# Performance work log

Hardware: AMD Instinct MI355X
Metric: run time of the kernel (lower is better)

The kernel has to match this reference:

```python
import jax, jax.numpy as jnp
import numpy as np


def _silu(x):
    return x * jax.nn.sigmoid(x)


def _mamba_dir(h, W_in, conv_w, conv_b, Wx, Wdt, bdt, A_log, Dp, W_out):
    """One unidirectional Mamba (v1) block. h: [B, L, Dm] -> [B, L, Dm]."""
    Bsz, L, Dm = h.shape
    Di = W_in.shape[0] // 2
    N = A_log.shape[1]
    K = conv_w.shape[1]
    dt_rank = Wdt.shape[1]
    # input projection -> x, z gates
    xz = jnp.einsum('bld,ed->ble', h, W_in)  # [B, L, 2*Di]
    x, z = xz[..., :Di], xz[..., Di:]
    # causal depthwise conv over time
    xc = jnp.transpose(x, (0, 2, 1))  # [B, Di, L]
    xc = jax.lax.conv_general_dilated(
        xc, conv_w[:, None, :], window_strides=(1,), padding=[(K - 1, 0)],
        dimension_numbers=('NCH', 'OIH', 'NCH'), feature_group_count=Di)
    x = _silu(jnp.transpose(xc, (0, 2, 1)) + conv_b[None, None, :])  # [B, L, Di]
    # data-dependent dt, B, C
    x_dbl = jnp.einsum('bld,ed->ble', x, Wx)  # [B, L, dt_rank + 2N]
    dt = x_dbl[..., :dt_rank]
    Bm = x_dbl[..., dt_rank:dt_rank + N]      # [B, L, N]
    Cm = x_dbl[..., dt_rank + N:]             # [B, L, N]
    dt = jax.nn.softplus(jnp.einsum('blr,dr->bld', dt, Wdt) + bdt)  # [B, L, Di]
    A = -jnp.exp(A_log)                       # [Di, N]
    # ZOH discretization
    dA = jnp.exp(dt[..., None] * A)                     # [B, L, Di, N]
    dBx = (dt * x)[..., None] * Bm[:, :, None, :]       # [B, L, Di, N]

    def step(hc, inp):
        dA_t, dBx_t, C_t = inp
        hc = dA_t * hc + dBx_t                          # [B, Di, N]
        return hc, jnp.einsum('bdn,bn->bd', hc, C_t)

    h0 = jnp.zeros((Bsz, Di, N), dtype=x.dtype)
    _, ys = jax.lax.scan(step, h0, (jnp.moveaxis(dA, 1, 0),
                                    jnp.moveaxis(dBx, 1, 0),
                                    jnp.moveaxis(Cm, 1, 0)))
    y = jnp.moveaxis(ys, 0, 1) + x * Dp                  # [B, L, Di]
    y = y * _silu(z)
    return jnp.einsum('bld,ed->ble', y, W_out)           # [B, L, Dm]


def setup_inputs() -> dict:
    key = jax.random.key(0)
    ks = jax.random.split(key, 16)
    B, L, Dm = 1, 2048, 1024
    Di, N, Kc, R = 2048, 16, 4, 64
    s = 0.02
    inp = {
        'hidden_states': jax.random.normal(ks[0], (B, L, Dm), jnp.float32),
        'W_in':  jax.random.normal(ks[1], (2 * Di, Dm), jnp.float32) * s,
        'W_out': jax.random.normal(ks[2], (Dm, Di), jnp.float32) * s,
    }
    a_log = jnp.log(jnp.broadcast_to(jnp.arange(1, N + 1, dtype=jnp.float32), (Di, N)))
    for i, d in enumerate(['fwd', 'rev']):
        o = 3 + 6 * i
        inp[f'conv_w_{d}'] = jax.random.normal(ks[o + 0], (Di, Kc), jnp.float32) * 0.2
        inp[f'conv_b_{d}'] = jnp.zeros((Di,), jnp.float32)
        inp[f'Wx_{d}']     = jax.random.normal(ks[o + 1], (R + 2 * N, Di), jnp.float32) * s
        inp[f'Wdt_{d}']    = jax.random.normal(ks[o + 2], (Di, R), jnp.float32) * s
        inp[f'bdt_{d}']    = jnp.full((Di,), -4.6, jnp.float32)  # softplus ~ 0.01
        inp[f'A_log_{d}']  = a_log
        inp[f'D_{d}']      = jnp.ones((Di,), jnp.float32)
    return inp


def reference(hidden_states, W_in, W_out,
              conv_w_fwd, conv_b_fwd, Wx_fwd, Wdt_fwd, bdt_fwd, A_log_fwd, D_fwd,
              conv_w_rev, conv_b_rev, Wx_rev, Wdt_rev, bdt_rev, A_log_rev, D_rev):
    out = _mamba_dir(hidden_states, W_in, conv_w_fwd, conv_b_fwd, Wx_fwd,
                     Wdt_fwd, bdt_fwd, A_log_fwd, D_fwd, W_out)
    h_rev = jnp.flip(hidden_states, axis=-2)
    out_rev = _mamba_dir(h_rev, W_in, conv_w_rev, conv_b_rev, Wx_rev,
                         Wdt_rev, bdt_rev, A_log_rev, D_rev, W_out)
    return out + jnp.flip(out_rev, axis=-2)
```

## Files before the change

### kernel.cpp

```cpp
#include <hip/hip_runtime.h>

#define L_LEN 2048
#define DM 1024
#define DI 2048
#define NS 16
#define KC 4
#define RR 64
#define XS 128
#define SPK 8
#define CH2 128
#define TCH2 (L_LEN / CH2)

typedef __attribute__((ext_vector_type(8))) short bf16x8;
typedef __attribute__((ext_vector_type(4))) float f32x4;

__device__ __forceinline__ float silu_f(float v) { return v / (1.f + __expf(-v)); }

__device__ __forceinline__ float exp2_f(float x) {
  float r;
  asm("v_exp_f32 %0, %1" : "=v"(r) : "v"(x));
  return r;
}

__device__ __forceinline__ unsigned short f2bf(float f) {
  unsigned int u = __float_as_uint(f);
  u = (u + 0x7FFFu + ((u >> 16) & 1u)) >> 16;
  return (unsigned short)u;
}
__device__ __forceinline__ float bf2f(unsigned short u) {
  return __uint_as_float((unsigned int)u << 16);
}

#define GLOAD_LDS16(gptr, lptr)                                                \
  __builtin_amdgcn_global_load_lds(                                            \
      (const __attribute__((address_space(1))) void*)(gptr),                   \
      (__attribute__((address_space(3))) void*)(lptr), 16, 0, 0)

template <int BM, int EPI, int KSPLIT>
__global__ __launch_bounds__(256) void gemm_bf16(
    const unsigned short* __restrict__ A, const unsigned short* __restrict__ B,
    void* __restrict__ Cv, void* __restrict__ Cv2, int M, int N, int K,
    size_t zsA, size_t zsB, size_t zsC,
    const float* __restrict__ biasf, const float* __restrict__ biasr)
{
  constexpr int MF = BM / 32;
  constexpr int WM = BM / 2;
  A += (size_t)blockIdx.z * zsA;
  B += (size_t)blockIdx.z * zsB;
  __shared__ unsigned short smem[(BM + 128) * 32];
  unsigned short* As = smem;
  unsigned short* Bs = smem + BM * 32;
  const int tid = threadIdx.x;
  const int wid = tid >> 6;
  const int lane = tid & 63;
  const int bm = blockIdx.x * BM;
  const int bn = (KSPLIT > 1) ? 0 : blockIdx.y * 128;
  int kbeg = 0, kend = K;
  if (KSPLIT > 1) {
    int kl = K / KSPLIT;
    kbeg = blockIdx.y * kl; kend = kbeg + kl;
  }
  const int wm = wid >> 1, wn = wid & 1;
  const int arow = tid >> 2;
  const int swz_kel = (((tid & 3) ^ ((tid >> 3) & 3)) << 3);
  const int qa = (((lane >> 4) ^ ((lane >> 1) & 3)) << 4);
  const int frow = lane & 15;

  f32x4 acc[MF][4];
#pragma unroll
  for (int mi = 0; mi < MF; ++mi)
#pragma unroll
    for (int ni = 0; ni < 4; ++ni) acc[mi][ni] = 0.f;

  const unsigned short* Ab = A + (size_t)bm * K + swz_kel;
  const unsigned short* Bb = B + (size_t)bn * K + swz_kel;

  for (int k0 = kbeg; k0 < kend; k0 += 32) {
#pragma unroll
    for (int i = 0; i < BM / 64; ++i)
      GLOAD_LDS16(Ab + (size_t)(i * 64 + arow) * K + k0,
                  (char*)As + i * 4096 + wid * 1024);
#pragma unroll
    for (int i = 0; i < 2; ++i)
      GLOAD_LDS16(Bb + (size_t)(i * 64 + arow) * K + k0,
                  (char*)Bs + i * 4096 + wid * 1024);
    __syncthreads();
    bf16x8 af[MF], bfr[4];
#pragma unroll
    for (int mi = 0; mi < MF; ++mi)
      af[mi] = *(const bf16x8*)((const char*)As + (wm * WM + mi * 16 + frow) * 64 + qa);
#pragma unroll
    for (int ni = 0; ni < 4; ++ni)
      bfr[ni] = *(const bf16x8*)((const char*)Bs + (wn * 64 + ni * 16 + frow) * 64 + qa);
#pragma unroll
    for (int mi = 0; mi < MF; ++mi)
#pragma unroll
      for (int ni = 0; ni < 4; ++ni)
        acc[mi][ni] = __builtin_amdgcn_mfma_f32_16x16x32_bf16(
            af[mi], bfr[ni], acc[mi][ni], 0, 0, 0);
    __syncthreads();
  }
  const int crow0 = bm + wm * WM + ((lane >> 4) << 2);
  const int ccol0 = bn + wn * 64 + frow;
  if (EPI == 1) {
    unsigned short* Cu = (unsigned short*)Cv + (size_t)blockIdx.z * zsC;
    const float* bias = blockIdx.z ? biasr : biasf;
    float bn4[4];
#pragma unroll
    for (int ni = 0; ni < 4; ++ni) bn4[ni] = bias[ccol0 + ni * 16];
#pragma unroll
    for (int mi = 0; mi < MF; ++mi)
#pragma unroll
      for (int ni = 0; ni < 4; ++ni)
#pragma unroll
        for (int v = 0; v < 4; ++v) {
          float val = acc[mi][ni][v] + bn4[ni];
          float sp = (val > 20.f) ? val : __logf(1.f + __expf(val));
          Cu[(size_t)(crow0 + mi * 16 + v) * N + ccol0 + ni * 16] = f2bf(sp);
        }
  } else if (EPI == 2) {
    unsigned short* Co = (bn < DI) ? (unsigned short*)Cv : (unsigned short*)Cv2;
    const int cbase = (bn < DI) ? 0 : DI;
#pragma unroll
    for (int mi = 0; mi < MF; ++mi)
#pragma unroll
      for (int ni = 0; ni < 4; ++ni)
#pragma unroll
        for (int v = 0; v < 4; ++v)
          Co[(size_t)(crow0 + mi * 16 + v) * DI + ccol0 + ni * 16 - cbase] =
              f2bf(acc[mi][ni][v]);
  } else {
    float* Cf = (float*)Cv + (size_t)blockIdx.z * zsC;
    if (KSPLIT > 1) Cf += (size_t)blockIdx.y * 2 * M * 128;
#pragma unroll
    for (int mi = 0; mi < MF; ++mi)
#pragma unroll
      for (int ni = 0; ni < 4; ++ni)
#pragma unroll
        for (int v = 0; v < 4; ++v)
          Cf[(size_t)(crow0 + mi * 16 + v) * N + ccol0 + ni * 16] = acc[mi][ni][v];
  }
}

__global__ __launch_bounds__(256) void cast_all(
    const float* __restrict__ Wxf, const float* __restrict__ Wxr,
    const float* __restrict__ Wdtf, const float* __restrict__ Wdtr,
    const float* __restrict__ W_out, const float* __restrict__ h,
    const float* __restrict__ W_in,
    unsigned short* __restrict__ Wxpad, unsigned short* __restrict__ wdtb,
    unsigned short* __restrict__ wob, unsigned short* __restrict__ hb)
{
  int idx = (blockIdx.x * 256 + threadIdx.x) * 4;
  const int N0 = 2 * XS * DI;
  const int N1 = N0 + 2 * DI * RR;
  const int N2 = N1 + DM * DI;
  const int N3 = N2 + L_LEN * DM;
  float4 v;
  ushort4 o = {0, 0, 0, 0};
  if (idx < N0) {
    int dir = idx >> 18;
    int rem = idx & ((1 << 18) - 1);
    int row = rem >> 11;
    if (row < 96) {
      v = *(const float4*)((dir ? Wxr : Wxf) + (size_t)row * DI + (rem & (DI - 1)));
      o.x = f2bf(v.x); o.y = f2bf(v.y); o.z = f2bf(v.z); o.w = f2bf(v.w);
    }
    *(ushort4*)(Wxpad + idx) = o;
    return;
  }
  unsigned short* dst;
  const float* src;
  int j;
  if (idx < N1)      { j = idx - N0; int dir = j >> 17;
                       src = (dir ? Wdtr : Wdtf) + (j & ((1 << 17) - 1)); dst = wdtb + j; }
  else if (idx < N2) { j = idx - N1; src = W_out + j; dst = wob + j; }
  else if (idx < N3) { j = idx - N2; src = h + j;     dst = hb + j; }
  else               { j = idx - N3; src = W_in + j;  dst = hb + (L_LEN * DM) + j; }
  v = *(const float4*)src;
  o.x = f2bf(v.x); o.y = f2bf(v.y); o.z = f2bf(v.z); o.w = f2bf(v.w);
  *(ushort4*)dst = o;
}

__global__ __launch_bounds__(256) void xdbl_reduce2(
    const float* __restrict__ part, float* __restrict__ xdbl2,
    unsigned short* __restrict__ xdblb)
{
  int idx = (blockIdx.x * 256 + threadIdx.x) * 4;
  f32x4 s = {0.f, 0.f, 0.f, 0.f};
#pragma unroll
  for (int sp = 0; sp < SPK; ++sp) {
    f32x4 p = *(const f32x4*)(part + (size_t)sp * 2 * L_LEN * XS + idx);
#pragma unroll
    for (int j = 0; j < 4; ++j) s[j] += p[j];
  }
  *(f32x4*)(xdbl2 + idx) = s;
  int col = idx & (XS - 1);
  if (col < RR) {
    int dr = idx >> 7;
    ushort4 o;
    o.x = f2bf(s[0]); o.y = f2bf(s[1]); o.z = f2bf(s[2]); o.w = f2bf(s[3]);
    *(ushort4*)(xdblb + (size_t)dr * RR + col) = o;
  }
}

__global__ __launch_bounds__(256) void conv_silu4(
    const unsigned short* __restrict__ xb,
    const float* __restrict__ wf, const float* __restrict__ bf,
    const float* __restrict__ wr, const float* __restrict__ br,
    unsigned short* __restrict__ xob)
{
  const int dir = blockIdx.y;
  const int idx = (blockIdx.x * 256 + threadIdx.x) * 4;
  const int d = idx & (DI - 1);
  const int t = idx >> 11;
  const float* w = dir ? wr : wf;
  const float* bb = dir ? br : bf;
  f32x4 wq[4];
#pragma unroll
  for (int j = 0; j < 4; ++j) wq[j] = *(const f32x4*)(w + (d + j) * KC);
  f32x4 s = {0.f, 0.f, 0.f, 0.f};
#pragma unroll
  for (int k = 0; k < KC; ++k) {
    int tt = t - (KC - 1) + k;
    if (tt >= 0) {
      int row = dir ? (L_LEN - 1 - tt) : tt;
      ushort4 xv = *(const ushort4*)(xb + (size_t)row * DI + d);
      s[0] = fmaf(wq[0][k], bf2f(xv.x), s[0]);
      s[1] = fmaf(wq[1][k], bf2f(xv.y), s[1]);
      s[2] = fmaf(wq[2][k], bf2f(xv.z), s[2]);
      s[3] = fmaf(wq[3][k], bf2f(xv.w), s[3]);
    }
  }
  f32x4 bv = *(const f32x4*)(bb + d);
  ushort4 o;
  o.x = f2bf(silu_f(s[0] + bv[0])); o.y = f2bf(silu_f(s[1] + bv[1]));
  o.z = f2bf(silu_f(s[2] + bv[2])); o.w = f2bf(silu_f(s[3] + bv[3]));
  *(ushort4*)(xob + (size_t)dir * L_LEN * DI + idx) = o;
}

__global__ __launch_bounds__(256) void scan_partial2(
    const unsigned short* __restrict__ dtb16, const unsigned short* __restrict__ xwb,
    const float* __restrict__ xdbl2,
    const float* __restrict__ Alogf, const float* __restrict__ Alogr,
    float* __restrict__ hch, float* __restrict__ sdtb)
{
  const int dir = blockIdx.z, c = blockIdx.y;
  const int d = blockIdx.x * 256 + threadIdx.x;
  const int t0 = c * TCH2;
  const unsigned short* dtp = dtb16 + (size_t)dir * L_LEN * DI + (size_t)t0 * DI + d;
  const unsigned short* xp  = xwb   + (size_t)dir * L_LEN * DI + (size_t)t0 * DI + d;
  const float* xdp = xdbl2 + (size_t)dir * L_LEN * XS + (size_t)t0 * XS;
  const float* Alog = (dir ? Alogr : Alogf) + (size_t)d * NS;
  f32x4 a4[4], h4[4];
#pragma unroll
  for (int g = 0; g < 4; ++g) {
    f32x4 al = *(const f32x4*)(Alog + g * 4);
#pragma unroll
    for (int j = 0; j < 4; ++j) a4[g][j] = -__expf(al[j]) * 1.44269504f;
    h4[g] = 0.f;
  }
  float sdt = 0.f;
#pragma unroll
  for (int tt = 0; tt < TCH2; ++tt) {
    float dtv = bf2f(*dtp);
    float xv  = bf2f(*xp);
    float dtx = dtv * xv;
    sdt += dtv;
#pragma unroll
    for (int g = 0; g < 4; ++g) {
      f32x4 Bv = *(const f32x4*)(xdp + RR + g * 4);
#pragma unroll
      for (int j = 0; j < 4; ++j)
        h4[g][j] = fmaf(exp2_f(dtv * a4[g][j]), h4[g][j], dtx * Bv[j]);
    }
    dtp += DI; xp += DI; xdp += XS;
  }
  float* hp = hch + ((((size_t)c * 2 + dir) * 4) * DI + d) * 4;
#pragma unroll
  for (int g = 0; g < 4; ++g) *(f32x4*)(hp + (size_t)g * DI * 4) = h4[g];
  sdtb[((size_t)c * 2 + dir) * DI + d] = sdt;
}

__global__ __launch_bounds__(256) void scan_combine2(
    float* __restrict__ hch, const float* __restrict__ sdtb,
    const float* __restrict__ Alogf, const float* __restrict__ Alogr)
{
  const int idx = blockIdx.x * 256 + threadIdx.x;
  const int dir = idx / (DI * NS);
  const int rem = idx - dir * (DI * NS);
  const int d = rem >> 4, n = rem & 15;
  const float* Alog = dir ? Alogr : Alogf;
  const float A2 = -__expf(Alog[rem]) * 1.44269504f;
  float H = 0.f;
  for (int c = 0; c < CH2; ++c) {
    size_t off = ((((size_t)c * 2 + dir) * 4 + (n >> 2)) * DI + d) * 4 + (n & 3);
    float hc = hch[off];
    hch[off] = H;
    H = fmaf(exp2_f(A2 * sdtb[((size_t)c * 2 + dir) * DI + d]), H, hc);
  }
}

__global__ __launch_bounds__(256) void scan_final3(
    const unsigned short* __restrict__ dtb16, const unsigned short* __restrict__ xwb,
    const float* __restrict__ xdbl2,
    const float* __restrict__ Alogf, const float* __restrict__ Alogr,
    const float* __restrict__ Df, const float* __restrict__ Dr,
    const float* __restrict__ Hin, const unsigned short* __restrict__ zb,
    unsigned short* __restrict__ yb)
{
  const int c = blockIdx.y;
  const int d = blockIdx.x * 256 + threadIdx.x;
  float ur[TCH2];
  {
    const int cr = CH2 - 1 - c;
    const int tr0 = cr * TCH2;
    const unsigned short* dtp = dtb16 + (size_t)L_LEN * DI + (size_t)tr0 * DI + d;
    const unsigned short* xp  = xwb   + (size_t)L_LEN * DI + (size_t)tr0 * DI + d;
    const float* xdp = xdbl2 + (size_t)L_LEN * XS + (size_t)tr0 * XS;
    const float* Alog = Alogr + (size_t)d * NS;
    const float Dp = Dr[d];
    f32x4 a4[4], h4[4];
#pragma unroll
    for (int g = 0; g < 4; ++g) {
      f32x4 al = *(const f32x4*)(Alog + g * 4);
      h4[g] = *(const f32x4*)(Hin + ((((size_t)cr * 2 + 1) * 4 + g) * DI + d) * 4);
#pragma unroll
      for (int j = 0; j < 4; ++j) a4[g][j] = -__expf(al[j]) * 1.44269504f;
    }
#pragma unroll
    for (int s = 0; s < TCH2; ++s) {
      float dtv = bf2f(*dtp);
      float xv  = bf2f(*xp);
      float dtx = dtv * xv;
      f32x4 p4 = {0.f, 0.f, 0.f, 0.f};
#pragma unroll
      for (int g = 0; g < 4; ++g) {
        f32x4 Bv = *(const f32x4*)(xdp + RR + g * 4);
        f32x4 Cv = *(const f32x4*)(xdp + RR + NS + g * 4);
#pragma unroll
        for (int j = 0; j < 4; ++j) {
          h4[g][j] = fmaf(exp2_f(dtv * a4[g][j]), h4[g][j], dtx * Bv[j]);
          p4[j] = fmaf(h4[g][j], Cv[j], p4[j]);
        }
      }
      float p = (p4[0] + p4[1]) + (p4[2] + p4[3]);
      ur[s] = fmaf(xv, Dp, p);
      dtp += DI; xp += DI; xdp += XS;
    }
  }
  {
    const int t0 = c * TCH2;
    const unsigned short* dtp = dtb16 + (size_t)t0 * DI + d;
    const unsigned short* xp  = xwb   + (size_t)t0 * DI + d;
    const float* xdp = xdbl2 + (size_t)t0 * XS;
    const unsigned short* zp = zb + (size_t)t0 * DI + d;
    unsigned short* yp = yb + (size_t)t0 * DI + d;
    const float* Alog = Alogf + (size_t)d * NS;
    const float Dp = Df[d];
    f32x4 a4[4], h4[4];
#pragma unroll
    for (int g = 0; g < 4; ++g) {
      f32x4 al = *(const f32x4*)(Alog + g * 4);
      h4[g] = *(const f32x4*)(Hin + ((((size_t)c * 2 + 0) * 4 + g) * DI + d) * 4);
#pragma unroll
      for (int j = 0; j < 4; ++j) a4[g][j] = -__expf(al[j]) * 1.44269504f;
    }
#pragma unroll
    for (int tt = 0; tt < TCH2; ++tt) {
      float dtv = bf2f(*dtp);
      float xv  = bf2f(*xp);
      float dtx = dtv * xv;
      f32x4 p4 = {0.f, 0.f, 0.f, 0.f};
#pragma unroll
      for (int g = 0; g < 4; ++g) {
        f32x4 Bv = *(const f32x4*)(xdp + RR + g * 4);
        f32x4 Cv = *(const f32x4*)(xdp + RR + NS + g * 4);
#pragma unroll
        for (int j = 0; j < 4; ++j) {
          h4[g][j] = fmaf(exp2_f(dtv * a4[g][j]), h4[g][j], dtx * Bv[j]);
          p4[j] = fmaf(h4[g][j], Cv[j], p4[j]);
        }
      }
      float p = (p4[0] + p4[1]) + (p4[2] + p4[3]);
      float uf = fmaf(xv, Dp, p);
      float u = uf + ur[TCH2 - 1 - tt];
      float z = bf2f(*zp);
      *yp = f2bf(u * silu_f(z));
      dtp += DI; xp += DI; xdp += XS; zp += DI; yp += DI;
    }
  }
}

extern "C" void kernel_launch(void* const* d_in, const int* in_sizes, int n_in,
                              void* d_out, int out_size, void* d_ws, size_t ws_size,
                              hipStream_t stream)
{
  const float* h     = (const float*)d_in[0];
  const float* W_in  = (const float*)d_in[1];
  const float* W_out = (const float*)d_in[2];
  const float* cwf   = (const float*)d_in[3];
  const float* cbf   = (const float*)d_in[4];
  const float* Wxf   = (const float*)d_in[5];
  const float* Wdtf  = (const float*)d_in[6];
  const float* bdtf  = (const float*)d_in[7];
  const float* Alogf = (const float*)d_in[8];
  const float* Df    = (const float*)d_in[9];
  const float* cwr   = (const float*)d_in[10];
  const float* cbr   = (const float*)d_in[11];
  const float* Wxr   = (const float*)d_in[12];
  const float* Wdtr  = (const float*)d_in[13];
  const float* bdtr  = (const float*)d_in[14];
  const float* Alogr = (const float*)d_in[15];
  const float* Dr    = (const float*)d_in[16];

  float* ws = (float*)d_ws;
  size_t o = 0;
  float* xb_f    = ws + o; o += (size_t)L_LEN * DI / 2;
  float* zb_f    = ws + o; o += (size_t)L_LEN * DI / 2;
  float* xwb_f   = ws + o; o += (size_t)L_LEN * DI;
  float* dtb_f   = ws + o; o += (size_t)L_LEN * DI;
  float* xdbl2   = ws + o; o += 2ull * L_LEN * XS;
  float* xdblb_f = ws + o; o += (size_t)L_LEN * RR;
  float* wdtb_f  = ws + o; o += (size_t)DI * RR;
  float* Wxpad_f = ws + o; o += (size_t)XS * DI;
  float* wob_f   = ws + o; o += (size_t)DM * DI / 2;
  float* yb_f    = ws + o; o += (size_t)L_LEN * DI / 2;
  float* R0      = ws + o; o += 8912896;
  if (ws_size < o * sizeof(float)) return;

  unsigned short* xb    = (unsigned short*)xb_f;
  unsigned short* zb    = (unsigned short*)zb_f;
  unsigned short* xwb   = (unsigned short*)xwb_f;
  unsigned short* dtb16 = (unsigned short*)dtb_f;
  unsigned short* xdblb = (unsigned short*)xdblb_f;
  unsigned short* wdtb  = (unsigned short*)wdtb_f;
  unsigned short* Wxpad = (unsigned short*)Wxpad_f;
  unsigned short* wob   = (unsigned short*)wob_f;
  unsigned short* yb    = (unsigned short*)yb_f;

  unsigned short* hb   = (unsigned short*)R0;
  float*          part = R0;
  float*          hch  = R0;
  float*          sdtb = R0 + 8388608;

  cast_all<<<(2 * XS * DI + 2 * DI * RR + DM * DI + L_LEN * DM + 2 * DI * DM) / 1024,
             256, 0, stream>>>(
      Wxf, Wxr, Wdtf, Wdtr, W_out, h, W_in, Wxpad, wdtb, wob, hb);

  gemm_bf16<128, 2, 1><<<dim3(L_LEN / 128, (2 * DI) / 128, 1), 256, 0, stream>>>(
      hb, hb + (size_t)L_LEN * DM, xb, zb, L_LEN, 2 * DI, DM, 0, 0, 0,
      nullptr, nullptr);

  conv_silu4<<<dim3(L_LEN * DI / 1024, 2), 256, 0, stream>>>(
      xb, cwf, cbf, cwr, cbr, xwb);

  gemm_bf16<128, 0, SPK><<<dim3(L_LEN / 128, SPK, 2), 256, 0, stream>>>(
      xwb, Wxpad, part, nullptr, L_LEN, XS, DI,
      (size_t)L_LEN * DI, (size_t)XS * DI, (size_t)L_LEN * XS,
      nullptr, nullptr);
  xdbl_reduce2<<<(2 * L_LEN * XS) / 1024, 256, 0, stream>>>(part, xdbl2, xdblb);

  gemm_bf16<128, 1, 1><<<dim3(L_LEN / 128, DI / 128, 2), 256, 0, stream>>>(
      xdblb, wdtb, dtb16, nullptr, L_LEN, DI, RR,
      (size_t)L_LEN * RR, (size_t)DI * RR, (size_t)L_LEN * DI,
      bdtf, bdtr);

  scan_partial2<<<dim3(DI / 256, CH2, 2), 256, 0, stream>>>(
      dtb16, xwb, xdbl2, Alogf, Alogr, hch, sdtb);
  scan_combine2<<<(2 * DI * NS) / 256, 256, 0, stream>>>(
      hch, sdtb, Alogf, Alogr);
  scan_final3<<<dim3(DI / 256, CH2, 1), 256, 0, stream>>>(
      dtb16, xwb, xdbl2, Alogf, Alogr, Df, Dr, hch, zb, yb);

  gemm_bf16<64, 0, 1><<<dim3(L_LEN / 64, DM / 128, 1), 256, 0, stream>>>(
      yb, wob, (float*)d_out, nullptr, L_LEN, DM, DI, 0, 0, 0, nullptr, nullptr);
}
```

Measured before the change: 192.9 us.

## Double-buffer GEMM LDS tiles and store split-K partials and chunk states in bf16

```diff
diff --git a/kernel.cpp b/kernel.cpp
--- a/kernel.cpp
+++ b/kernel.cpp
@@ -45,11 +45,10 @@
 {
   constexpr int MF = BM / 32;
   constexpr int WM = BM / 2;
+  constexpr int HALF = (BM + 128) * 32;
   A += (size_t)blockIdx.z * zsA;
   B += (size_t)blockIdx.z * zsB;
-  __shared__ unsigned short smem[(BM + 128) * 32];
-  unsigned short* As = smem;
-  unsigned short* Bs = smem + BM * 32;
+  __shared__ unsigned short smem[2 * HALF];
   const int tid = threadIdx.x;
   const int wid = tid >> 6;
   const int lane = tid & 63;
@@ -60,6 +59,7 @@
     int kl = K / KSPLIT;
     kbeg = blockIdx.y * kl; kend = kbeg + kl;
   }
+  const int nsteps = (kend - kbeg) >> 5;
   const int wm = wid >> 1, wn = wid & 1;
   const int arow = tid >> 2;
   const int swz_kel = (((tid & 3) ^ ((tid >> 3) & 3)) << 3);
@@ -75,30 +75,44 @@
   const unsigned short* Ab = A + (size_t)bm * K + swz_kel;
   const unsigned short* Bb = B + (size_t)bn * K + swz_kel;
 
-  for (int k0 = kbeg; k0 < kend; k0 += 32) {
+  auto STAGE = [&](int s, int buf) {
+    char* As = (char*)(smem + buf * HALF);
+    char* Bs = As + BM * 64;
+    const int k0 = kbeg + s * 32;
 #pragma unroll
     for (int i = 0; i < BM / 64; ++i)
       GLOAD_LDS16(Ab + (size_t)(i * 64 + arow) * K + k0,
-                  (char*)As + i * 4096 + wid * 1024);
+                  As + i * 4096 + wid * 1024);
 #pragma unroll
     for (int i = 0; i < 2; ++i)
       GLOAD_LDS16(Bb + (size_t)(i * 64 + arow) * K + k0,
-                  (char*)Bs + i * 4096 + wid * 1024);
-    __syncthreads();
+                  Bs + i * 4096 + wid * 1024);
+  };
+
+  STAGE(0, 0);
+  __syncthreads();
+  int cur = 0;
+  for (int s = 0; s < nsteps; ++s) {
+    if (s + 1 < nsteps) STAGE(s + 1, cur ^ 1);
+    const char* As = (const char*)(smem + cur * HALF);
+    const char* Bs = As + BM * 64;
     bf16x8 af[MF], bfr[4];
 #pragma unroll
     for (int mi = 0; mi < MF; ++mi)
-      af[mi] = *(const bf16x8*)((const char*)As + (wm * WM + mi * 16 + frow) * 64 + qa);
+      af[mi] = *(const bf16x8*)(As + (wm * WM + mi * 16 + frow) * 64 + qa);
 #pragma unroll
     for (int ni = 0; ni < 4; ++ni)
-      bfr[ni] = *(const bf16x8*)((const char*)Bs + (wn * 64 + ni * 16 + frow) * 64 + qa);
+      bfr[ni] = *(const bf16x8*)(Bs + (wn * 64 + ni * 16 + frow) * 64 + qa);
 #pragma unroll
     for (int mi = 0; mi < MF; ++mi)
 #pragma unroll
       for (int ni = 0; ni < 4; ++ni)
         acc[mi][ni] = __builtin_amdgcn_mfma_f32_16x16x32_bf16(
             af[mi], bfr[ni], acc[mi][ni], 0, 0, 0);
-    __syncthreads();
+    if (s + 1 < nsteps) {
+      __syncthreads();
+      cur ^= 1;
+    }
   }
   const int crow0 = bm + wm * WM + ((lane >> 4) << 2);
   const int ccol0 = bn + wn * 64 + frow;
@@ -129,9 +143,19 @@
         for (int v = 0; v < 4; ++v)
           Co[(size_t)(crow0 + mi * 16 + v) * DI + ccol0 + ni * 16 - cbase] =
               f2bf(acc[mi][ni][v]);
+  } else if (EPI == 3) {
+    unsigned short* Cu = (unsigned short*)Cv + (size_t)blockIdx.z * zsC +
+                         (size_t)blockIdx.y * 2 * M * 128;
+#pragma unroll
+    for (int mi = 0; mi < MF; ++mi)
+#pragma unroll
+      for (int ni = 0; ni < 4; ++ni)
+#pragma unroll
+        for (int v = 0; v < 4; ++v)
+          Cu[(size_t)(crow0 + mi * 16 + v) * N + ccol0 + ni * 16] =
+              f2bf(acc[mi][ni][v]);
   } else {
     float* Cf = (float*)Cv + (size_t)blockIdx.z * zsC;
-    if (KSPLIT > 1) Cf += (size_t)blockIdx.y * 2 * M * 128;
 #pragma unroll
     for (int mi = 0; mi < MF; ++mi)
 #pragma unroll
@@ -182,16 +206,15 @@
 }
 
 __global__ __launch_bounds__(256) void xdbl_reduce2(
-    const float* __restrict__ part, float* __restrict__ xdbl2,
+    const unsigned short* __restrict__ part, float* __restrict__ xdbl2,
     unsigned short* __restrict__ xdblb)
 {
   int idx = (blockIdx.x * 256 + threadIdx.x) * 4;
   f32x4 s = {0.f, 0.f, 0.f, 0.f};
 #pragma unroll
   for (int sp = 0; sp < SPK; ++sp) {
-    f32x4 p = *(const f32x4*)(part + (size_t)sp * 2 * L_LEN * XS + idx);
-#pragma unroll
-    for (int j = 0; j < 4; ++j) s[j] += p[j];
+    ushort4 p = *(const ushort4*)(part + (size_t)sp * 2 * L_LEN * XS + idx);
+    s[0] += bf2f(p.x); s[1] += bf2f(p.y); s[2] += bf2f(p.z); s[3] += bf2f(p.w);
   }
   *(f32x4*)(xdbl2 + idx) = s;
   int col = idx & (XS - 1);
@@ -242,7 +265,7 @@
     const unsigned short* __restrict__ dtb16, const unsigned short* __restrict__ xwb,
     const float* __restrict__ xdbl2,
     const float* __restrict__ Alogf, const float* __restrict__ Alogr,
-    float* __restrict__ hch, float* __restrict__ sdtb)
+    unsigned short* __restrict__ hch, float* __restrict__ sdtb)
 {
   const int dir = blockIdx.z, c = blockIdx.y;
   const int d = blockIdx.x * 256 + threadIdx.x;
@@ -275,14 +298,19 @@
     }
     dtp += DI; xp += DI; xdp += XS;
   }
-  float* hp = hch + ((((size_t)c * 2 + dir) * 4) * DI + d) * 4;
-#pragma unroll
-  for (int g = 0; g < 4; ++g) *(f32x4*)(hp + (size_t)g * DI * 4) = h4[g];
+  unsigned short* hp = hch + ((((size_t)c * 2 + dir) * 4) * DI + d) * 4;
+#pragma unroll
+  for (int g = 0; g < 4; ++g) {
+    ushort4 o;
+    o.x = f2bf(h4[g][0]); o.y = f2bf(h4[g][1]);
+    o.z = f2bf(h4[g][2]); o.w = f2bf(h4[g][3]);
+    *(ushort4*)(hp + (size_t)g * DI * 4) = o;
+  }
   sdtb[((size_t)c * 2 + dir) * DI + d] = sdt;
 }
 
 __global__ __launch_bounds__(256) void scan_combine2(
-    float* __restrict__ hch, const float* __restrict__ sdtb,
+    unsigned short* __restrict__ hch, const float* __restrict__ sdtb,
     const float* __restrict__ Alogf, const float* __restrict__ Alogr)
 {
   const int idx = blockIdx.x * 256 + threadIdx.x;
@@ -294,8 +322,8 @@
   float H = 0.f;
   for (int c = 0; c < CH2; ++c) {
     size_t off = ((((size_t)c * 2 + dir) * 4 + (n >> 2)) * DI + d) * 4 + (n & 3);
-    float hc = hch[off];
-    hch[off] = H;
+    float hc = bf2f(hch[off]);
+    hch[off] = f2bf(H);
     H = fmaf(exp2_f(A2 * sdtb[((size_t)c * 2 + dir) * DI + d]), H, hc);
   }
 }
@@ -305,7 +333,7 @@
     const float* __restrict__ xdbl2,
     const float* __restrict__ Alogf, const float* __restrict__ Alogr,
     const float* __restrict__ Df, const float* __restrict__ Dr,
-    const float* __restrict__ Hin, const unsigned short* __restrict__ zb,
+    const unsigned short* __restrict__ Hin, const unsigned short* __restrict__ zb,
     unsigned short* __restrict__ yb)
 {
   const int c = blockIdx.y;
@@ -323,7 +351,9 @@
 #pragma unroll
     for (int g = 0; g < 4; ++g) {
       f32x4 al = *(const f32x4*)(Alog + g * 4);
-      h4[g] = *(const f32x4*)(Hin + ((((size_t)cr * 2 + 1) * 4 + g) * DI + d) * 4);
+      ushort4 hv = *(const ushort4*)(Hin + ((((size_t)cr * 2 + 1) * 4 + g) * DI + d) * 4);
+      h4[g][0] = bf2f(hv.x); h4[g][1] = bf2f(hv.y);
+      h4[g][2] = bf2f(hv.z); h4[g][3] = bf2f(hv.w);
 #pragma unroll
       for (int j = 0; j < 4; ++j) a4[g][j] = -__expf(al[j]) * 1.44269504f;
     }
@@ -361,7 +391,9 @@
 #pragma unroll
     for (int g = 0; g < 4; ++g) {
       f32x4 al = *(const f32x4*)(Alog + g * 4);
-      h4[g] = *(const f32x4*)(Hin + ((((size_t)c * 2 + 0) * 4 + g) * DI + d) * 4);
+      ushort4 hv = *(const ushort4*)(Hin + ((((size_t)c * 2 + 0) * 4 + g) * DI + d) * 4);
+      h4[g][0] = bf2f(hv.x); h4[g][1] = bf2f(hv.y);
+      h4[g][2] = bf2f(hv.z); h4[g][3] = bf2f(hv.w);
 #pragma unroll
       for (int j = 0; j < 4; ++j) a4[g][j] = -__expf(al[j]) * 1.44269504f;
     }
@@ -425,7 +457,7 @@
   float* Wxpad_f = ws + o; o += (size_t)XS * DI;
   float* wob_f   = ws + o; o += (size_t)DM * DI / 2;
   float* yb_f    = ws + o; o += (size_t)L_LEN * DI / 2;
-  float* R0      = ws + o; o += 8912896;
+  float* R0      = ws + o; o += 4718592;
   if (ws_size < o * sizeof(float)) return;
 
   unsigned short* xb    = (unsigned short*)xb_f;
@@ -439,9 +471,9 @@
   unsigned short* yb    = (unsigned short*)yb_f;
 
   unsigned short* hb   = (unsigned short*)R0;
-  float*          part = R0;
-  float*          hch  = R0;
-  float*          sdtb = R0 + 8388608;
+  unsigned short* part = (unsigned short*)R0;
+  unsigned short* hch  = (unsigned short*)R0;
+  float*          sdtb = R0 + 4194304;
 
   cast_all<<<(2 * XS * DI + 2 * DI * RR + DM * DI + L_LEN * DM + 2 * DI * DM) / 1024,
              256, 0, stream>>>(
@@ -454,7 +486,7 @@
   conv_silu4<<<dim3(L_LEN * DI / 1024, 2), 256, 0, stream>>>(
       xb, cwf, cbf, cwr, cbr, xwb);
 
-  gemm_bf16<128, 0, SPK><<<dim3(L_LEN / 128, SPK, 2), 256, 0, stream>>>(
+  gemm_bf16<128, 3, SPK><<<dim3(L_LEN / 128, SPK, 2), 256, 0, stream>>>(
       xwb, Wxpad, part, nullptr, L_LEN, XS, DI,
       (size_t)L_LEN * DI, (size_t)XS * DI, (size_t)L_LEN * XS,
       nullptr, nullptr);
```

Result: faster. 176.2 us (-8.6%).
